# Kernel optimization log

Measured on AMD Instinct MI355X. Metric: run time of the kernel, lower is better.

The kernel has to match this reference:

```python
import jax, jax.numpy as jnp
import numpy as np
from jax import lax

B = 128

# ---- 4-qubit statevector helpers (RY + CNOT circuit is real-valued) ----

def _init_state(n):
    s = jnp.zeros((n, 2, 2, 2, 2), jnp.float32)
    return s.at[:, 0, 0, 0, 0].set(1.0)


def _ry(state, theta, wire):
    # RY(t) = [[cos t/2, -sin t/2],[sin t/2, cos t/2]]; theta: scalar or [N]
    s = jnp.moveaxis(state, wire + 1, 1)
    c = jnp.cos(theta * 0.5)
    sn = jnp.sin(theta * 0.5)
    if jnp.ndim(theta) > 0:
        c = c.reshape(-1, 1, 1, 1)
        sn = sn.reshape(-1, 1, 1, 1)
    a, b = s[:, 0], s[:, 1]
    s = jnp.stack([c * a - sn * b, sn * a + c * b], axis=1)
    return jnp.moveaxis(s, 1, wire + 1)


def _cnot(state, ctrl, tgt):
    s = jnp.moveaxis(state, [ctrl + 1, tgt + 1], [1, 2])
    s = jnp.concatenate([s[:, :1], jnp.flip(s[:, 1:], axis=2)], axis=1)
    return jnp.moveaxis(s, [1, 2], [ctrl + 1, tgt + 1])


def _random_layer(state, thetas):
    for i in range(4):
        state = _ry(state, thetas[i], i)
        state = _cnot(state, i, (i + 1) % 4)
    return state


def _measure_z(state, wire):
    p = jnp.moveaxis(state, wire + 1, 1) ** 2
    p = p.reshape(p.shape[0], 2, -1).sum(-1)
    return p[:, 0] - p[:, 1]


def setup_inputs() -> dict:
    key = jax.random.key(0)
    ks = jax.random.split(key, 12)

    def n(k, shape, scale):
        return jax.random.normal(k, shape, jnp.float32) * scale

    return {
        "x": jax.random.normal(ks[0], (B, 3, 249, 249), jnp.float32),
        "conv1_w": n(ks[1], (6, 3, 5, 5), 0.1),
        "conv1_b": jnp.zeros((6,), jnp.float32),
        "conv2_w": n(ks[2], (15, 6, 3, 3), 0.1),
        "conv2_b": jnp.zeros((15,), jnp.float32),
        "fc1_w": n(ks[3], (120, 55815), 1.0 / np.sqrt(55815.0)),
        "fc1_b": jnp.zeros((120,), jnp.float32),
        "fc2_w": n(ks[4], (84, 120), 1.0 / np.sqrt(120.0)),
        "fc2_b": jnp.zeros((84,), jnp.float32),
        "fc3_w": n(ks[5], (1, 84), 1.0 / np.sqrt(84.0)),
        "fc3_b": jnp.zeros((1,), jnp.float32),
        "head_thetas": jax.random.uniform(ks[6], (4,), jnp.float32, 0.0, 2.0 * np.pi),
        "qf_thetas": jax.random.uniform(ks[7], (4,), jnp.float32, 0.0, 2.0 * np.pi),
        "lin_w": n(ks[8], (1, 784), 1.0 / np.sqrt(784.0)),
        "lin_b": jnp.zeros((1,), jnp.float32),
    }


def reference(x, conv1_w, conv1_b, conv2_w, conv2_b, fc1_w, fc1_b, fc2_w, fc2_b,
              fc3_w, fc3_b, head_thetas, qf_thetas, lin_w, lin_b):
    bsz = x.shape[0]

    def conv(y, w, b, stride):
        y = lax.conv_general_dilated(y, w, (stride, stride), [(1, 1), (1, 1)],
                                     dimension_numbers=("NCHW", "OIHW", "NCHW"))
        return y + b[None, :, None, None]

    def pool(y):  # MaxPool2d(kernel=2, stride=1)
        return lax.reduce_window(y, -jnp.inf, lax.max, (1, 1, 2, 2), (1, 1, 1, 1), "VALID")

    # ---- conv branch (dropout = identity in eval) ----
    h = pool(jax.nn.relu(conv(x, conv1_w, conv1_b, 2)))          # [B,6,123,123]
    h = pool(jax.nn.relu(conv(h, conv2_w, conv2_b, 2)))          # [B,15,61,61]
    h = h.reshape(bsz, -1)                                        # [B,55815]
    h = jax.nn.relu(h @ fc1_w.T + fc1_b)
    h = jax.nn.relu(h @ fc2_w.T + fc2_b)
    logit = (h @ fc3_w.T + fc3_b)[:, 0]                           # [B]
    st = _init_state(bsz)
    st = _ry(st, logit, 0)
    st = _random_layer(st, head_thetas)
    probs_conv = jax.nn.sigmoid(_measure_z(st, 0))[:, None]       # [B,1]

    # ---- quanvolution branch ----
    gray = x.mean(axis=1, keepdims=True)                          # [B,1,249,249]
    g = jax.image.resize(gray, (bsz, 1, 28, 28), method="linear")[:, 0]
    # 2x2 patches, row-major, element order [tl, tr, bl, br]
    patches = g.reshape(bsz, 14, 2, 14, 2).transpose(0, 1, 3, 2, 4).reshape(bsz * 196, 4)
    st = _init_state(bsz * 196)
    for w in range(4):
        st = _ry(st, patches[:, w], w)
    st = _random_layer(st, qf_thetas)
    feats = jnp.stack([_measure_z(st, w) for w in range(4)], axis=1).reshape(bsz, 784)
    probs_q = jax.nn.sigmoid(feats @ lin_w.T + lin_b)             # [B,1]

    probs = (probs_conv + probs_q) * 0.5
    return jnp.concatenate([probs, 1.0 - probs], axis=-1)         # [B,2]
```

## Files before the change

### kernel.cpp

```cpp
#include <hip/hip_runtime.h>
#include <math.h>

#define DEV static __device__ __forceinline__

template <int W>
DEV void q_ry(float s[16], float th) {
  float c = cosf(th * 0.5f), sn = sinf(th * 0.5f);
  constexpr int m = 8 >> W;
#pragma unroll
  for (int i = 0; i < 16; ++i) {
    if (!(i & m)) {
      float a = s[i], b = s[i | m];
      s[i] = c * a - sn * b;
      s[i | m] = sn * a + c * b;
    }
  }
}
template <int C, int T>
DEV void q_cnot(float s[16]) {
  constexpr int mc = 8 >> C, mt = 8 >> T;
#pragma unroll
  for (int i = 0; i < 16; ++i) {
    if ((i & mc) && !(i & mt)) {
      float t = s[i]; s[i] = s[i | mt]; s[i | mt] = t;
    }
  }
}
template <int W>
DEV float q_mz(const float s[16]) {
  constexpr int m = 8 >> W;
  float p = 0.f;
#pragma unroll
  for (int i = 0; i < 16; ++i) p += (i & m) ? -s[i] * s[i] : s[i] * s[i];
  return p;
}
DEV void q_layer(float s[16], const float* __restrict__ th) {
  q_ry<0>(s, th[0]); q_cnot<0, 1>(s);
  q_ry<1>(s, th[1]); q_cnot<1, 2>(s);
  q_ry<2>(s, th[2]); q_cnot<2, 3>(s);
  q_ry<3>(s, th[3]); q_cnot<3, 0>(s);
}

__global__ void k_wre(const float* __restrict__ c1w, float* __restrict__ wre1) {
  int t = blockIdx.x * 256 + threadIdx.x;
  if (t < 450) {
    int g = t / 30, rem = t % 30;
    int ci = g / 5, ky = g % 5, kx = rem / 6, co = rem % 6;
    wre1[t] = c1w[co * 75 + ci * 25 + ky * 5 + kx];
  }
}

DEV int c1_rowbase(int row) { return row * 39 + ((row >> 1) & 1); }

__global__ __launch_bounds__(256, 4) void k_conv1(const float* __restrict__ x,
                                                  const float* __restrict__ wre1,
                                                  const float* __restrict__ bia,
                                                  float* __restrict__ out) {
  __shared__ float smem[4800];
  float (*ct)[42][19] = (float (*)[42][19])smem;
  int b = blockIdx.z;
  int PY0 = blockIdx.y * 41, PX0 = blockIdx.x * 16;
  int iy0 = PY0 * 2 - 1, ix0 = PX0 * 2 - 1;
  int tid = threadIdx.x;
  const float* xb = x + (size_t)b * 186003;
  int r = tid / 6, seg = tid - 6 * (tid / 6);
  float acc[6][3];
#pragma unroll
  for (int co = 0; co < 6; ++co) {
    float bv = bia[co];
#pragma unroll
    for (int c = 0; c < 3; ++c) acc[co][c] = bv;
  }
#pragma unroll 1
  for (int ci = 0; ci < 3; ++ci) {
    if (ci) __syncthreads();
    const float* xci = xb + ci * 62001;
#pragma unroll
    for (int s = 0; s < 14; ++s) {
      int idx = s * 256 + tid;
      bool ok = idx < 3393;
      int rr = idx / 39, cc = idx - rr * 39;
      int iy = iy0 + rr, ix = ix0 + cc;
      float v = 0.f;
      if (ok && cc < 37 && (unsigned)iy < 249u && (unsigned)ix < 249u)
        v = xci[iy * 249 + ix];
      if (ok && cc < 37) smem[c1_rowbase(rr) + cc] = v;
    }
    __syncthreads();
    if (tid < 252) {
#pragma unroll
      for (int ky = 0; ky < 5; ++ky) {
        const float* xrow = &smem[c1_rowbase(2 * r + ky) + 6 * seg];
        float xv[10];
#pragma unroll
        for (int j = 0; j < 10; ++j) xv[j] = xrow[j];
        const float* wp = wre1 + (ci * 5 + ky) * 30;
        float wr[30];
#pragma unroll
        for (int j = 0; j < 30; ++j) wr[j] = wp[j];
#pragma unroll
        for (int c = 0; c < 3; ++c)
#pragma unroll
          for (int kx = 0; kx < 5; ++kx)
#pragma unroll
            for (int co = 0; co < 6; ++co)
              acc[co][c] += xv[2 * c + kx] * wr[kx * 6 + co];
      }
    }
  }
  __syncthreads();
  if (tid < 252) {
#pragma unroll
    for (int co = 0; co < 6; ++co)
#pragma unroll
      for (int c = 0; c < 3; ++c)
        if (3 * seg + c < 17) ct[co][r][3 * seg + c] = acc[co][c];
  }
  __syncthreads();
#pragma unroll
  for (int co2 = 0; co2 < 6; ++co2) {
    for (int j = tid; j < 41 * 16; j += 256) {
      int pr = j >> 4, pc = j & 15;
      float m = fmaxf(fmaxf(ct[co2][pr][pc], ct[co2][pr][pc + 1]),
                      fmaxf(ct[co2][pr + 1][pc], ct[co2][pr + 1][pc + 1]));
      out[((size_t)(b * 6 + co2) * 123 + PY0 + pr) * 128 + PX0 + pc] = fmaxf(m, 0.f);
    }
  }
}

__global__ __launch_bounds__(256, 4) void k_conv2(const float* __restrict__ in,
                                                  const float* __restrict__ w,
                                                  const float* __restrict__ bia,
                                                  float* __restrict__ out) {
  __shared__ float smem[6 * 35 * 36];
  float (*xs)[35][36] = (float (*)[35][36])smem;
  float (*ct)[17][18] = (float (*)[17][18])smem;
  int b = blockIdx.z;
  int py0 = blockIdx.y * 16, px0 = blockIdx.x * 16;
  int iy0 = py0 * 2 - 1, ix0 = px0 * 2 - 1;
  int tid = threadIdx.x;
  const float* ib = in + (size_t)b * 94464;
  for (int idx = tid; idx < 6 * 35 * 36; idx += 256) {
    int ci = idx / 1260, rem = idx % 1260, rr = rem / 36, cc = rem % 36;
    int iy = iy0 + rr, ix = ix0 + cc;
    float v = 0.f;
    if (cc < 35 && (unsigned)iy < 123u && (unsigned)ix < 123u)
      v = ib[ci * 15744 + iy * 128 + ix];
    xs[ci][rr][cc] = v;
  }
  __syncthreads();
  int co = tid % 15, ty = tid / 15;
  float acc[17];
  if (tid < 255) {
    float bv = bia[co];
#pragma unroll
    for (int t = 0; t < 17; ++t) acc[t] = bv;
#pragma unroll
    for (int ci = 0; ci < 6; ++ci) {
      float wreg[9];
#pragma unroll
      for (int j = 0; j < 9; ++j) wreg[j] = w[co * 54 + ci * 9 + j];
#pragma unroll
      for (int ky = 0; ky < 3; ++ky) {
        const float* xrow = &xs[ci][2 * ty + ky][0];
        float xv[36];
#pragma unroll
        for (int j = 0; j < 18; ++j) {
          float2 t2 = *reinterpret_cast<const float2*>(&xrow[2 * j]);
          xv[2 * j] = t2.x; xv[2 * j + 1] = t2.y;
        }
#pragma unroll
        for (int tx = 0; tx < 17; ++tx)
#pragma unroll
          for (int kx = 0; kx < 3; ++kx)
            acc[tx] += xv[2 * tx + kx] * wreg[ky * 3 + kx];
      }
    }
  }
  __syncthreads();
  if (tid < 255) {
#pragma unroll
    for (int tx = 0; tx < 17; ++tx) ct[co][ty][tx] = acc[tx];
  }
  __syncthreads();
  for (int i = tid; i < 15 * 16 * 16; i += 256) {
    int co2 = i / 256, rem = i % 256, pr = rem / 16, pc = rem % 16;
    int py = py0 + pr, px = px0 + pc;
    if (py < 61 && px < 61) {
      float m = fmaxf(fmaxf(ct[co2][pr][pc], ct[co2][pr][pc + 1]),
                      fmaxf(ct[co2][pr + 1][pc], ct[co2][pr + 1][pc + 1]));
      out[(size_t)b * 55815 + co2 * 3721 + py * 61 + px] = fmaxf(m, 0.f);
    }
  }
}

#define KFC 55815
#define NCHUNK 1745
#define FC1_BLOCKS 512
__global__ __launch_bounds__(256) void k_fc1(const float* __restrict__ h,
                                             const float* __restrict__ w,
                                             float* __restrict__ partial) {
  __shared__ float hs[128][33];
  __shared__ float wsd[120][33];
  int tid = threadIdx.x;
  int tb = tid & 31;
  int bo = tid >> 5;
  float acc[4][15];
#pragma unroll
  for (int j = 0; j < 4; ++j)
#pragma unroll
    for (int oo = 0; oo < 15; ++oo) acc[j][oo] = 0.f;

  for (int ch = blockIdx.x; ch < NCHUNK; ch += FC1_BLOCKS) {
    int k0 = ch * 32;
    for (int idx = tid; idx < 128 * 32; idx += 256) {
      int bb = idx >> 5, kk = idx & 31;
      int k = k0 + kk;
      hs[bb][kk] = (k < KFC) ? h[(size_t)bb * KFC + k] : 0.f;
    }
    for (int idx = tid; idx < 120 * 32; idx += 256) {
      int oo = idx >> 5, kk = idx & 31;
      int k = k0 + kk;
      wsd[oo][kk] = (k < KFC) ? w[(size_t)oo * KFC + k] : 0.f;
    }
    __syncthreads();
#pragma unroll 4
    for (int kk = 0; kk < 32; ++kk) {
      float hv[4], wv[15];
#pragma unroll
      for (int j = 0; j < 4; ++j) hv[j] = hs[tb + 32 * j][kk];
#pragma unroll
      for (int oo = 0; oo < 15; ++oo) wv[oo] = wsd[bo * 15 + oo][kk];
#pragma unroll
      for (int j = 0; j < 4; ++j)
#pragma unroll
        for (int oo = 0; oo < 15; ++oo) acc[j][oo] += hv[j] * wv[oo];
    }
    __syncthreads();
  }
  float* pg = partial + (size_t)blockIdx.x * 15360;
#pragma unroll
  for (int j = 0; j < 4; ++j) {
    int b = tb + 32 * j;
#pragma unroll
    for (int oo = 0; oo < 15; ++oo) pg[b * 120 + bo * 15 + oo] = acc[j][oo];
  }
}

__global__ __launch_bounds__(256) void k_fc1_reduce(const float* __restrict__ partial,
                                                    const float* __restrict__ bias,
                                                    float* __restrict__ outv) {
  int i = blockIdx.x * 256 + threadIdx.x;
  if (i >= 15360) return;
  float a = bias[i % 120];
  for (int g = 0; g < FC1_BLOCKS; ++g) a += partial[(size_t)g * 15360 + i];
  outv[i] = fmaxf(a, 0.f);
}

__global__ __launch_bounds__(128) void k_head(const float* __restrict__ fc1o,
                                              const float* __restrict__ w2,
                                              const float* __restrict__ b2,
                                              const float* __restrict__ w3,
                                              const float* __restrict__ b3,
                                              const float* __restrict__ hth,
                                              float* __restrict__ probs_conv) {
  __shared__ float h1[120];
  __shared__ float h2[84];
  int b = blockIdx.x, tid = threadIdx.x;
  if (tid < 120) h1[tid] = fc1o[b * 120 + tid];
  __syncthreads();
  if (tid < 84) {
    float a = b2[tid];
    for (int k = 0; k < 120; ++k) a += h1[k] * w2[tid * 120 + k];
    h2[tid] = fmaxf(a, 0.f);
  }
  __syncthreads();
  if (tid == 0) {
    float lg = b3[0];
    for (int j = 0; j < 84; ++j) lg += h2[j] * w3[j];
    float s[16];
#pragma unroll
    for (int i = 0; i < 16; ++i) s[i] = 0.f;
    s[0] = 1.f;
    q_ry<0>(s, lg);
    q_layer(s, hth);
    float z = q_mz<0>(s);
    probs_conv[b] = 1.f / (1.f + expf(-z));
  }
}

DEV void resize_win(int o, int& i0, int& i1, float& sf, float& inorm) {
  const float invs = 249.0f / 28.0f;
  sf = ((float)o + 0.5f) * invs - 0.5f;
  i0 = (int)ceilf(sf - invs); if (i0 < 0) i0 = 0;
  i1 = (int)floorf(sf + invs); if (i1 > 248) i1 = 248;
  float nrm = 0.f;
  for (int i = i0; i <= i1; ++i)
    nrm += fmaxf(0.f, 1.f - fabsf(sf - (float)i) * (28.0f / 249.0f));
  inorm = 1.f / nrm;
}

__global__ __launch_bounds__(256) void k_resize_rows(const float* __restrict__ x,
                                                     float* __restrict__ tmp) {
  int b = blockIdx.x / 28, oy = blockIdx.x % 28;
  int ix = threadIdx.x;
  if (ix >= 249) return;
  int i0, i1; float sf, inorm;
  resize_win(oy, i0, i1, sf, inorm);
  const float* xb = x + (size_t)b * 186003;
  float acc = 0.f;
  for (int iy = i0; iy <= i1; ++iy) {
    float wv = fmaxf(0.f, 1.f - fabsf(sf - (float)iy) * (28.0f / 249.0f)) * inorm;
    float gr = (xb[iy * 249 + ix] + xb[62001 + iy * 249 + ix] +
                xb[124002 + iy * 249 + ix]) * (1.0f / 3.0f);
    acc += wv * gr;
  }
  tmp[((size_t)b * 28 + oy) * 249 + ix] = acc;
}

__global__ __launch_bounds__(256) void k_quanv(const float* __restrict__ tmp,
                                               const float* __restrict__ qth,
                                               const float* __restrict__ lw,
                                               float* __restrict__ qpart) {
  __shared__ float g[392];
  __shared__ float red[4];
  int bid = blockIdx.x;
  int b = bid >> 1, half = bid & 1;
  int tid = threadIdx.x;
  for (int idx = tid; idx < 392; idx += 256) {
    int ly = idx / 28, ox = idx % 28;
    int oy = 14 * half + ly;
    int i0, i1; float sf, inorm;
    resize_win(ox, i0, i1, sf, inorm);
    const float* tr = tmp + ((size_t)b * 28 + oy) * 249;
    float acc = 0.f;
    for (int i = i0; i <= i1; ++i)
      acc += fmaxf(0.f, 1.f - fabsf(sf - (float)i) * (28.0f / 249.0f)) * inorm * tr[i];
    g[idx] = acc;
  }
  __syncthreads();
  float part = 0.f;
  if (tid < 98) {
    int pl = tid / 14, pj = tid % 14;
    int pi = 7 * half + pl;
    float v0 = g[(2 * pl) * 28 + 2 * pj];
    float v1 = g[(2 * pl) * 28 + 2 * pj + 1];
    float v2 = g[(2 * pl + 1) * 28 + 2 * pj];
    float v3 = g[(2 * pl + 1) * 28 + 2 * pj + 1];
    float s[16];
#pragma unroll
    for (int i = 0; i < 16; ++i) s[i] = 0.f;
    s[0] = 1.f;
    q_ry<0>(s, v0); q_ry<1>(s, v1); q_ry<2>(s, v2); q_ry<3>(s, v3);
    q_layer(s, qth);
    float z0 = q_mz<0>(s), z1 = q_mz<1>(s), z2 = q_mz<2>(s), z3 = q_mz<3>(s);
    const float* lwp = lw + (pi * 14 + pj) * 4;
    part = z0 * lwp[0] + z1 * lwp[1] + z2 * lwp[2] + z3 * lwp[3];
  }
#pragma unroll
  for (int off = 32; off > 0; off >>= 1) part += __shfl_down(part, off, 64);
  if ((tid & 63) == 0) red[tid >> 6] = part;
  __syncthreads();
  if (tid == 0) qpart[bid] = red[0] + red[1] + red[2] + red[3];
}

__global__ __launch_bounds__(128) void k_final(const float* __restrict__ qpart,
                                               const float* __restrict__ lb,
                                               const float* __restrict__ probs_conv,
                                               float* __restrict__ out) {
  int b = threadIdx.x;
  float tot = qpart[2 * b] + qpart[2 * b + 1] + lb[0];
  float pq = 1.f / (1.f + expf(-tot));
  float pr = 0.5f * (probs_conv[b] + pq);
  out[b * 2 + 0] = pr;
  out[b * 2 + 1] = 1.f - pr;
}

extern "C" void kernel_launch(void* const* d_in, const int* in_sizes, int n_in,
                              void* d_out, int out_size, void* d_ws, size_t ws_size,
                              hipStream_t stream) {
  const float* x   = (const float*)d_in[0];
  const float* c1w = (const float*)d_in[1];
  const float* c1b = (const float*)d_in[2];
  const float* c2w = (const float*)d_in[3];
  const float* c2b = (const float*)d_in[4];
  const float* f1w = (const float*)d_in[5];
  const float* f1b = (const float*)d_in[6];
  const float* f2w = (const float*)d_in[7];
  const float* f2b = (const float*)d_in[8];
  const float* f3w = (const float*)d_in[9];
  const float* f3b = (const float*)d_in[10];
  const float* hth = (const float*)d_in[11];
  const float* qth = (const float*)d_in[12];
  const float* lw  = (const float*)d_in[13];
  const float* lb  = (const float*)d_in[14];
  float* out = (float*)d_out;
  char* ws = (char*)d_ws;

  float* pool1   = (float*)(ws);
  float* partial = (float*)(ws);
  float* tmp     = (float*)(ws + 33554432);
  float* h       = (float*)(ws + 48365568);
  float* fc1o    = (float*)(ws + 76942848);
  float* pconv   = (float*)(ws + 77004288);
  float* wre1    = (float*)(ws + 77004800);
  float* qpart   = (float*)(ws + 77009848);

  k_wre<<<dim3(2), 256, 0, stream>>>(c1w, wre1);
  k_conv1<<<dim3(8, 3, 128), 256, 0, stream>>>(x, wre1, c1b, pool1);
  k_conv2<<<dim3(4, 4, 128), 256, 0, stream>>>(pool1, c2w, c2b, h);
  k_fc1<<<dim3(FC1_BLOCKS), 256, 0, stream>>>(h, f1w, partial);
  k_fc1_reduce<<<dim3(60), 256, 0, stream>>>(partial, f1b, fc1o);
  k_head<<<dim3(128), 128, 0, stream>>>(fc1o, f2w, f2b, f3w, f3b, hth, pconv);
  k_resize_rows<<<dim3(128 * 28), 256, 0, stream>>>(x, tmp);
  k_quanv<<<dim3(256), 256, 0, stream>>>(tmp, qth, lw, qpart);
  k_final<<<dim3(1), 128, 0, stream>>>(qpart, lb, pconv, out);
}
```

Before: 260.3 us.

## Retile fc1 to 128 threads with 8x15 register blocks; scatter-based row resize

The fc1 GEMV-style kernel now runs 128 threads per block, each accumulating 8 batch rows by 15 outputs. It reads weights from shared memory as float2, over 768 blocks instead of 512. The row-resize kernel is rewritten so each input row is read once and scattered into at most two output rows through shared-memory accumulators, instead of re-reading overlapping windows for every output row. This cuts redundant global reads of x in the resize and raises register reuse in fc1. The cost is higher register pressure, fewer threads per block, and more partial sums for the reduce kernel to process.

```diff
diff --git a/kernel.cpp b/kernel.cpp
--- a/kernel.cpp
+++ b/kernel.cpp
@@ -196,52 +196,59 @@
 
 #define KFC 55815
 #define NCHUNK 1745
-#define FC1_BLOCKS 512
-__global__ __launch_bounds__(256) void k_fc1(const float* __restrict__ h,
+#define FC1_BLOCKS 768
+__global__ __launch_bounds__(128) void k_fc1(const float* __restrict__ h,
                                              const float* __restrict__ w,
                                              float* __restrict__ partial) {
   __shared__ float hs[128][33];
-  __shared__ float wsd[120][33];
+  __shared__ float wsd[120][36];
   int tid = threadIdx.x;
-  int tb = tid & 31;
-  int bo = tid >> 5;
-  float acc[4][15];
-#pragma unroll
-  for (int j = 0; j < 4; ++j)
+  int tb = tid & 15;
+  int bo = tid >> 4;
+  float acc[8][15];
+#pragma unroll
+  for (int j = 0; j < 8; ++j)
 #pragma unroll
     for (int oo = 0; oo < 15; ++oo) acc[j][oo] = 0.f;
 
   for (int ch = blockIdx.x; ch < NCHUNK; ch += FC1_BLOCKS) {
     int k0 = ch * 32;
-    for (int idx = tid; idx < 128 * 32; idx += 256) {
+#pragma unroll
+    for (int s = 0; s < 32; ++s) {
+      int idx = s * 128 + tid;
       int bb = idx >> 5, kk = idx & 31;
       int k = k0 + kk;
       hs[bb][kk] = (k < KFC) ? h[(size_t)bb * KFC + k] : 0.f;
     }
-    for (int idx = tid; idx < 120 * 32; idx += 256) {
+#pragma unroll
+    for (int s = 0; s < 30; ++s) {
+      int idx = s * 128 + tid;
       int oo = idx >> 5, kk = idx & 31;
       int k = k0 + kk;
       wsd[oo][kk] = (k < KFC) ? w[(size_t)oo * KFC + k] : 0.f;
     }
     __syncthreads();
-#pragma unroll 4
-    for (int kk = 0; kk < 32; ++kk) {
-      float hv[4], wv[15];
-#pragma unroll
-      for (int j = 0; j < 4; ++j) hv[j] = hs[tb + 32 * j][kk];
-#pragma unroll
-      for (int oo = 0; oo < 15; ++oo) wv[oo] = wsd[bo * 15 + oo][kk];
-#pragma unroll
-      for (int j = 0; j < 4; ++j)
-#pragma unroll
-        for (int oo = 0; oo < 15; ++oo) acc[j][oo] += hv[j] * wv[oo];
+#pragma unroll
+    for (int kk2 = 0; kk2 < 16; ++kk2) {
+      float2 wq[15];
+#pragma unroll
+      for (int oo = 0; oo < 15; ++oo)
+        wq[oo] = *reinterpret_cast<const float2*>(&wsd[bo * 15 + oo][2 * kk2]);
+#pragma unroll
+      for (int j = 0; j < 8; ++j) {
+        float h0 = hs[tb + 16 * j][2 * kk2];
+        float h1 = hs[tb + 16 * j][2 * kk2 + 1];
+#pragma unroll
+        for (int oo = 0; oo < 15; ++oo)
+          acc[j][oo] += h0 * wq[oo].x + h1 * wq[oo].y;
+      }
     }
     __syncthreads();
   }
   float* pg = partial + (size_t)blockIdx.x * 15360;
 #pragma unroll
-  for (int j = 0; j < 4; ++j) {
-    int b = tb + 32 * j;
+  for (int j = 0; j < 8; ++j) {
+    int b = tb + 16 * j;
 #pragma unroll
     for (int oo = 0; oo < 15; ++oo) pg[b * 120 + bo * 15 + oo] = acc[j][oo];
   }
@@ -300,22 +307,49 @@
   inorm = 1.f / nrm;
 }
 
-__global__ __launch_bounds__(256) void k_resize_rows(const float* __restrict__ x,
-                                                     float* __restrict__ tmp) {
-  int b = blockIdx.x / 28, oy = blockIdx.x % 28;
-  int ix = threadIdx.x;
-  if (ix >= 249) return;
-  int i0, i1; float sf, inorm;
-  resize_win(oy, i0, i1, sf, inorm);
+__global__ __launch_bounds__(256) void k_resize1(const float* __restrict__ x,
+                                                 float* __restrict__ tmp) {
+  __shared__ float accs[4][28][64];
+  __shared__ float sf_t[28], inorm_t[28];
+  int b = blockIdx.x >> 2, cg = blockIdx.x & 3;
+  int tid = threadIdx.x;
+  int iysub = tid >> 6, lane = tid & 63;
+  int col = cg * 64 + lane;
+  bool colok = col < 249;
+  for (int i = tid; i < 4 * 28 * 64; i += 256) ((float*)accs)[i] = 0.f;
+  if (tid < 28) {
+    int i0, i1; float sf, inm;
+    resize_win(tid, i0, i1, sf, inm);
+    sf_t[tid] = sf; inorm_t[tid] = inm;
+  }
+  __syncthreads();
   const float* xb = x + (size_t)b * 186003;
-  float acc = 0.f;
-  for (int iy = i0; iy <= i1; ++iy) {
-    float wv = fmaxf(0.f, 1.f - fabsf(sf - (float)iy) * (28.0f / 249.0f)) * inorm;
-    float gr = (xb[iy * 249 + ix] + xb[62001 + iy * 249 + ix] +
-                xb[124002 + iy * 249 + ix]) * (1.0f / 3.0f);
-    acc += wv * gr;
-  }
-  tmp[((size_t)b * 28 + oy) * 249 + ix] = acc;
+  const float S = 28.0f / 249.0f;
+  for (int it = 0; it < 63; ++it) {
+    int iy = it * 4 + iysub;
+    if (iy < 249 && colok) {
+      int off = iy * 249 + col;
+      float gray = (xb[off] + xb[62001 + off] + xb[124002 + off]) * (1.0f / 3.0f);
+      float u = ((float)iy + 0.5f) * S;
+      int oyh = (int)floorf(u + 0.5f);
+#pragma unroll
+      for (int d = 0; d < 2; ++d) {
+        int oy = oyh - d;
+        if (oy >= 0 && oy < 28) {
+          float wv = fmaxf(0.f, 1.f - fabsf(sf_t[oy] - (float)iy) * S) * inorm_t[oy];
+          accs[iysub][oy][lane] += wv * gray;
+        }
+      }
+    }
+  }
+  __syncthreads();
+  for (int i = tid; i < 28 * 64; i += 256) {
+    int oy = i >> 6, c2 = i & 63;
+    int colw = cg * 64 + c2;
+    if (colw < 249)
+      tmp[((size_t)b * 28 + oy) * 249 + colw] =
+          accs[0][oy][c2] + accs[1][oy][c2] + accs[2][oy][c2] + accs[3][oy][c2];
+  }
 }
 
 __global__ __launch_bounds__(256) void k_quanv(const float* __restrict__ tmp,
@@ -409,10 +443,10 @@
   k_wre<<<dim3(2), 256, 0, stream>>>(c1w, wre1);
   k_conv1<<<dim3(8, 3, 128), 256, 0, stream>>>(x, wre1, c1b, pool1);
   k_conv2<<<dim3(4, 4, 128), 256, 0, stream>>>(pool1, c2w, c2b, h);
-  k_fc1<<<dim3(FC1_BLOCKS), 256, 0, stream>>>(h, f1w, partial);
+  k_fc1<<<dim3(FC1_BLOCKS), 128, 0, stream>>>(h, f1w, partial);
   k_fc1_reduce<<<dim3(60), 256, 0, stream>>>(partial, f1b, fc1o);
   k_head<<<dim3(128), 128, 0, stream>>>(fc1o, f2w, f2b, f3w, f3b, hth, pconv);
-  k_resize_rows<<<dim3(128 * 28), 256, 0, stream>>>(x, tmp);
+  k_resize1<<<dim3(512), 256, 0, stream>>>(x, tmp);
   k_quanv<<<dim3(256), 256, 0, stream>>>(tmp, qth, lw, qpart);
   k_final<<<dim3(1), 128, 0, stream>>>(qpart, lb, pconv, out);
 }
```

New measurement: 488.3 us. 87.6% more time.
